# Kernel optimization log

Hardware: AMD Instinct MI355X
Metric: run time of the kernel (lower is better)

Reference implementation:

```python
import jax, jax.numpy as jnp
import numpy as np

B, S, T = 4, 1024, 1024
CTX, QIN, C, H = 1024, 1024, 1024, 16
HD = C // H  # per-head channels


def setup_inputs() -> dict:
    key = jax.random.key(0)
    ks = jax.random.split(key, 12)
    s = 0.02
    return {
        "query": jax.random.normal(ks[0], (B, S, QIN), jnp.float32),
        "key": jax.random.normal(ks[1], (B, T, CTX), jnp.float32),
        "value": jax.random.normal(ks[2], (B, T, CTX), jnp.float32),
        "mask": jax.random.randint(ks[3], (B, S, T), 0, 2).astype(bool),
        "Wq": jax.random.normal(ks[4], (C, QIN), jnp.float32) * s,
        "bq": jax.random.normal(ks[5], (C,), jnp.float32) * s,
        "Wk": jax.random.normal(ks[6], (C, CTX), jnp.float32) * s,
        "bk": jax.random.normal(ks[7], (C,), jnp.float32) * s,
        "Wv": jax.random.normal(ks[8], (C, CTX), jnp.float32) * s,
        "bv": jax.random.normal(ks[9], (C,), jnp.float32) * s,
        "Wo": jax.random.normal(ks[10], (C, C), jnp.float32) * s,
        "bo": jax.random.normal(ks[11], (C,), jnp.float32) * s,
    }


def reference(query, key, value, mask, Wq, bq, Wk, bk, Wv, bv, Wo, bo):
    b, s, _ = query.shape
    t = key.shape[1]
    c = Wq.shape[0]
    h, hd = H, c // H
    q = (query @ Wq.T + bq).reshape(b, s, h, hd)
    k = (key @ Wk.T + bk).reshape(b, t, h, hd)
    v = (value @ Wv.T + bv).reshape(b, t, h, hd)
    # [B,H,S,T] scores, scaled by 1/sqrt(head_dim)
    score = jnp.einsum('bshd,bthd->bhst', q, k) * (hd ** -0.5)
    # masked_fill_(~mask[:, None, 0:1], -inf): mask key positions via row 0
    score = jnp.where(mask[:, None, 0:1], score, -jnp.inf)
    weights = jax.nn.softmax(score, axis=-1)
    out = jnp.einsum('bhst,bthd->bshd', weights, v).reshape(b, s, c)
    out = out @ Wo.T + bo
    out = out * mask[..., 0:1].astype(out.dtype)
    return out
```

## Files before the change

### kernel.cpp

```cpp
#include <hip/hip_runtime.h>
#include <stdint.h>

#define Bb  4
#define Ss  1024
#define Tt  1024
#define Cc  1024
#define Hh  16
#define HDd 64
#define Kk  1024

typedef __bf16 bf16;
typedef __bf16 bf16x8 __attribute__((ext_vector_type(8)));
typedef float  f32x4  __attribute__((ext_vector_type(4)));
typedef __attribute__((address_space(1))) uint32_t gu32;
typedef __attribute__((address_space(3))) uint32_t lu32;

__device__ __forceinline__ void load_lds16(const bf16* g, bf16* l) {
    __builtin_amdgcn_global_load_lds((gu32*)g, (lu32*)l, 16, 0, 0);
}

#define BARRIER_LDS() do {                                    \
    asm volatile("s_waitcnt lgkmcnt(0)" ::: "memory");        \
    __builtin_amdgcn_s_barrier();                             \
} while (0)

#define BARRIER_VM() do {                                     \
    asm volatile("s_waitcnt vmcnt(0)" ::: "memory");          \
    __builtin_amdgcn_s_barrier();                             \
} while (0)

__global__ void cvt8(const float* __restrict__ s0, const float* __restrict__ s1,
                     const float* __restrict__ s2, const float* __restrict__ s3,
                     const float* __restrict__ s4, const float* __restrict__ s5,
                     const float* __restrict__ s6,
                     bf16* __restrict__ d0, bf16* __restrict__ d1,
                     bf16* __restrict__ d2, bf16* __restrict__ d3,
                     bf16* __restrict__ d4, bf16* __restrict__ d5,
                     bf16* __restrict__ d6)
{
    const float* s; bf16* d; int n;
    switch (blockIdx.y) {
        case 0: s = s0; d = d0; n = Bb * Ss * Kk; break;
        case 1: s = s1; d = d1; n = Bb * Ss * Kk; break;
        case 2: s = s2; d = d2; n = Bb * Ss * Kk; break;
        case 3: s = s3; d = d3; n = Cc * Kk; break;
        case 4: s = s4; d = d4; n = Cc * Kk; break;
        case 5: s = s5; d = d5; n = Cc * Kk; break;
        default: s = s6; d = d6; n = Cc * Kk; break;
    }
    const int i = (blockIdx.x * blockDim.x + threadIdx.x) * 8;
    if (i >= n) return;
    const float4 a = *(const float4*)(s + i);
    const float4 c = *(const float4*)(s + i + 4);
    bf16x8 o;
    o[0] = (bf16)a.x; o[1] = (bf16)a.y; o[2] = (bf16)a.z; o[3] = (bf16)a.w;
    o[4] = (bf16)c.x; o[5] = (bf16)c.y; o[6] = (bf16)c.z; o[7] = (bf16)c.w;
    *(bf16x8*)(d + i) = o;
}

__device__ __forceinline__ void mainloop_128x64_pf(
    const bf16* __restrict__ Ab, const bf16* __restrict__ Wb,
    bf16* As, bf16* Bs, f32x4 acc[4][2])
{
    const int tid  = threadIdx.x;
    const int wid  = tid >> 6;
    const int lane = tid & 63;
    const int l16  = lane & 15;
    const int quad = lane >> 4;
    const int wm   = wid >> 1;
    const int wn   = wid & 1;
    const int r8   = lane >> 3;
    const int ssw  = ((lane & 7) ^ r8) * 8;

    auto stage = [&](int k0) {
#pragma unroll
        for (int p = 0; p < 4; p++) {
            const int rb = wid * 32 + p * 8;
            load_lds16(Ab + (size_t)(rb + r8) * Kk + k0 + ssw, As + rb * 64);
        }
#pragma unroll
        for (int p = 0; p < 2; p++) {
            const int rb = wid * 16 + p * 8;
            load_lds16(Wb + (size_t)(rb + r8) * Kk + k0 + ssw, Bs + rb * 64);
        }
    };

    stage(0);
    BARRIER_VM();

    for (int k0 = 0; k0 < Kk; k0 += 64) {
        bf16x8 af[2][4], bw[2][2];
#pragma unroll
        for (int kh = 0; kh < 2; kh++) {
#pragma unroll
            for (int i = 0; i < 4; i++)
                af[kh][i] = *(const bf16x8*)(As + (wm * 64 + i * 16 + l16) * 64 +
                                             (((kh * 4 + quad) ^ (l16 & 7)) * 8));
#pragma unroll
            for (int j = 0; j < 2; j++)
                bw[kh][j] = *(const bf16x8*)(Bs + (wn * 32 + j * 16 + l16) * 64 +
                                             (((kh * 4 + quad) ^ (l16 & 7)) * 8));
        }
        BARRIER_LDS();
        if (k0 + 64 < Kk) stage(k0 + 64);
#pragma unroll
        for (int kh = 0; kh < 2; kh++)
#pragma unroll
            for (int i = 0; i < 4; i++)
#pragma unroll
                for (int j = 0; j < 2; j++)
                    acc[i][j] = __builtin_amdgcn_mfma_f32_16x16x32_bf16(af[kh][i], bw[kh][j], acc[i][j], 0, 0, 0);
        BARRIER_VM();
    }
}

__global__ __launch_bounds__(256)
void gemm_qkv(const bf16* __restrict__ Aq, const bf16* __restrict__ Ak, const bf16* __restrict__ Av,
              const bf16* __restrict__ Wq, const bf16* __restrict__ Wk, const bf16* __restrict__ Wv,
              const float* __restrict__ bq, const float* __restrict__ bk, const float* __restrict__ bv,
              bf16* __restrict__ Oq, bf16* __restrict__ Ok, bf16* __restrict__ Ov)
{
    __shared__ __align__(16) bf16 As[128 * 64];
    __shared__ __align__(16) bf16 Bs[64 * 64];
    const int z = blockIdx.z;
    const bf16*  A    = (z == 0) ? Aq : (z == 1) ? Ak : Av;
    const bf16*  W    = (z == 0) ? Wq : (z == 1) ? Wk : Wv;
    const float* bias = (z == 0) ? bq : (z == 1) ? bk : bv;
    bf16*        O    = (z == 0) ? Oq : (z == 1) ? Ok : Ov;

    f32x4 acc[4][2];
    const f32x4 z4 = {0.f, 0.f, 0.f, 0.f};
#pragma unroll
    for (int i = 0; i < 4; i++)
#pragma unroll
        for (int j = 0; j < 2; j++) acc[i][j] = z4;

    mainloop_128x64_pf(A + (size_t)blockIdx.x * 128 * Kk,
                       W + (size_t)blockIdx.y * 64 * Kk, As, Bs, acc);

    const int tid = threadIdx.x;
    const int wid = tid >> 6, lane = tid & 63;
    const int l16 = lane & 15, quad = lane >> 4;
    const int wm = wid >> 1, wn = wid & 1;
    const int row0 = blockIdx.x * 128 + wm * 64;
    const int col0 = blockIdx.y * 64 + wn * 32;
#pragma unroll
    for (int j = 0; j < 2; j++) {
        const int col = col0 + j * 16 + l16;
        const float bj = bias[col];
        const int h = col >> 6, d = col & 63;
#pragma unroll
        for (int i = 0; i < 4; i++) {
#pragma unroll
            for (int r = 0; r < 4; r++) {
                const int row = row0 + i * 16 + quad * 4 + r;
                const int b = row >> 10, s = row & 1023;
                const bf16 val = (bf16)(acc[i][j][r] + bj);
                if (z == 2) {
                    Ov[((size_t)((b * Hh + h) * HDd + d)) * Tt + s] = val;
                } else {
                    O[((size_t)(b * Hh + h) * Ss + s) * HDd + d] = val;
                }
            }
        }
    }
}

__global__ __launch_bounds__(256)
void gemm_out(const bf16* __restrict__ A, const bf16* __restrict__ W,
              const float* __restrict__ bias, const int* __restrict__ mask,
              float* __restrict__ out)
{
    __shared__ __align__(16) bf16 As[128 * 64];
    __shared__ __align__(16) bf16 Bs[64 * 64];
    f32x4 acc[4][2];
    const f32x4 z4 = {0.f, 0.f, 0.f, 0.f};
#pragma unroll
    for (int i = 0; i < 4; i++)
#pragma unroll
        for (int j = 0; j < 2; j++) acc[i][j] = z4;

    mainloop_128x64_pf(A + (size_t)blockIdx.x * 128 * Kk,
                       W + (size_t)blockIdx.y * 64 * Kk, As, Bs, acc);

    const int tid = threadIdx.x;
    const int wid = tid >> 6, lane = tid & 63;
    const int l16 = lane & 15, quad = lane >> 4;
    const int wm = wid >> 1, wn = wid & 1;
    const int row0 = blockIdx.x * 128 + wm * 64;
    const int col0 = blockIdx.y * 64 + wn * 32;
#pragma unroll
    for (int j = 0; j < 2; j++) {
        const int col = col0 + j * 16 + l16;
        const float bj = bias[col];
#pragma unroll
        for (int i = 0; i < 4; i++) {
#pragma unroll
            for (int r = 0; r < 4; r++) {
                const int row = row0 + i * 16 + quad * 4 + r;
                const float mval = (mask[(size_t)row * Tt] != 0) ? 1.f : 0.f;
                out[(size_t)row * Cc + col] = (acc[i][j][r] + bj) * mval;
            }
        }
    }
}

__global__ __launch_bounds__(256, 4)
void attn(const bf16* __restrict__ Q, const bf16* __restrict__ Kp, const bf16* __restrict__ Vt,
          const int* __restrict__ mask, bf16* __restrict__ X)
{
    __shared__ __align__(16) bf16 Ks[64 * 64];
    __shared__ __align__(16) bf16 Vs[64 * 64];
    __shared__ __align__(16) bf16 Ps[4][16 * 72];
    const int g   = blockIdx.x;
    const int xcd = g & 7, idx = g >> 3;
    const int bh  = xcd * 8 + (idx >> 4);
    const int qblk = idx & 15;
    const int b = bh >> 4, h = bh & 15;
    const int tid = threadIdx.x, wid = tid >> 6, lane = tid & 63;
    const int l16 = lane & 15, quad = lane >> 4;
    const bf16* Qbh = Q  + (size_t)bh * Ss * HDd;
    const bf16* Kbh = Kp + (size_t)bh * Tt * HDd;
    const bf16* Vbh = Vt + (size_t)bh * HDd * Tt;
    const int*  mb  = mask + (size_t)b * Ss * Tt;
    const int q0 = qblk * 64 + wid * 16;
    bf16* Psw = &Ps[wid][0];

    const bf16x8 qf0 = *(const bf16x8*)(Qbh + (size_t)(q0 + l16) * HDd + quad * 8);
    const bf16x8 qf1 = *(const bf16x8*)(Qbh + (size_t)(q0 + l16) * HDd + 32 + quad * 8);

    float ls[4];
    f32x4 o[4];
    const f32x4 z4 = {0.f, 0.f, 0.f, 0.f};
#pragma unroll
    for (int r = 0; r < 4; r++) ls[r] = 0.f;
#pragma unroll
    for (int dblk = 0; dblk < 4; dblk++) o[dblk] = z4;

    const int srow = lane >> 3;
    const int schk = lane & 7;
    const int sswz = (schk ^ srow) * 8;
    const int c80 = wid * 2, c81 = wid * 2 + 1;

    const bf16* kg0 = Kbh + (size_t)(c80 * 8 + srow) * HDd + sswz;
    const bf16* kg1 = Kbh + (size_t)(c81 * 8 + srow) * HDd + sswz;
    const bf16* vg0 = Vbh + (size_t)(c80 * 8 + srow) * Tt + sswz;
    const bf16* vg1 = Vbh + (size_t)(c81 * 8 + srow) * Tt + sswz;
    bf16* kd0 = Ks + c80 * 512 + lane * 8;
    bf16* kd1 = Ks + c81 * 512 + lane * 8;
    bf16* vd0 = Vs + c80 * 512 + lane * 8;
    bf16* vd1 = Vs + c81 * 512 + lane * 8;

    bf16x8 ka0, ka1, va0, va1;
    bf16x8 kb0, kb1, vb0, vb1;
    int mA0, mA1, mA2, mA3, mB0, mB1, mB2, mB3;

#define LOADA(KT) do { const int _kt = (KT);                          \
    ka0 = *(const bf16x8*)(kg0 + (size_t)_kt * HDd);                  \
    ka1 = *(const bf16x8*)(kg1 + (size_t)_kt * HDd);                  \
    va0 = *(const bf16x8*)(vg0 + _kt);                                \
    va1 = *(const bf16x8*)(vg1 + _kt);                                \
    mA0 = mb[_kt + l16];      mA1 = mb[_kt + 16 + l16];               \
    mA2 = mb[_kt + 32 + l16]; mA3 = mb[_kt + 48 + l16]; } while (0)
#define LOADB(KT) do { const int _kt = (KT);                          \
    kb0 = *(const bf16x8*)(kg0 + (size_t)_kt * HDd);                  \
    kb1 = *(const bf16x8*)(kg1 + (size_t)_kt * HDd);                  \
    vb0 = *(const bf16x8*)(vg0 + _kt);                                \
    vb1 = *(const bf16x8*)(vg1 + _kt);                                \
    mB0 = mb[_kt + l16];      mB1 = mb[_kt + 16 + l16];               \
    mB2 = mb[_kt + 32 + l16]; mB3 = mb[_kt + 48 + l16]; } while (0)
#define STOREA() do {                                                 \
    *(bf16x8*)kd0 = ka0; *(bf16x8*)kd1 = ka1;                         \
    *(bf16x8*)vd0 = va0; *(bf16x8*)vd1 = va1; } while (0)
#define STOREB() do {                                                 \
    *(bf16x8*)kd0 = kb0; *(bf16x8*)kd1 = kb1;                         \
    *(bf16x8*)vd0 = vb0; *(bf16x8*)vd1 = vb1; } while (0)

    auto compute = [&](int m0, int m1, int m2, int m3) {
        f32x4 sc[4];
#pragma unroll
        for (int nb = 0; nb < 4; nb++) sc[nb] = z4;
#pragma unroll
        for (int nb = 0; nb < 4; nb++) {
            const bf16* krow = Ks + (nb * 16 + l16) * 64;
            const bf16x8 kf0 = *(const bf16x8*)(krow + ((quad       ^ (l16 & 7)) * 8));
            const bf16x8 kf1 = *(const bf16x8*)(krow + (((4 + quad) ^ (l16 & 7)) * 8));
            sc[nb] = __builtin_amdgcn_mfma_f32_16x16x32_bf16(qf0, kf0, sc[nb], 0, 0, 0);
            sc[nb] = __builtin_amdgcn_mfma_f32_16x16x32_bf16(qf1, kf1, sc[nb], 0, 0, 0);
        }

        const int mm[4] = {m0, m1, m2, m3};
#pragma unroll
        for (int nb = 0; nb < 4; nb++) {
            const float madd = mm[nb] ? 0.f : -1e30f;
#pragma unroll
            for (int r = 0; r < 4; r++) {
                const float p = __expf(sc[nb][r] * 0.125f + madd);
                ls[r] += p;
                Psw[(quad * 4 + r) * 72 + nb * 16 + l16] = (bf16)p;
            }
        }

#pragma unroll
        for (int kh = 0; kh < 2; kh++) {
            const bf16x8 pf = *(const bf16x8*)(Psw + l16 * 72 + kh * 32 + quad * 8);
#pragma unroll
            for (int dblk = 0; dblk < 4; dblk++) {
                const bf16x8 vf = *(const bf16x8*)(Vs + (dblk * 16 + l16) * 64 +
                                                   (((kh * 4 + quad) ^ (l16 & 7)) * 8));
                o[dblk] = __builtin_amdgcn_mfma_f32_16x16x32_bf16(pf, vf, o[dblk], 0, 0, 0);
            }
        }
    };

    LOADA(0);

    for (int kt = 0; kt < Tt; kt += 128) {
        BARRIER_LDS();
        LOADB(kt + 64);
        STOREA();
        BARRIER_LDS();
        compute(mA0, mA1, mA2, mA3);

        BARRIER_LDS();
        LOADA((kt + 128 < Tt) ? (kt + 128) : (Tt - 64));
        STOREB();
        BARRIER_LDS();
        compute(mB0, mB1, mB2, mB3);
    }
#undef LOADA
#undef LOADB
#undef STOREA
#undef STOREB

#pragma unroll
    for (int off = 1; off <= 8; off <<= 1)
#pragma unroll
        for (int r = 0; r < 4; r++)
            ls[r] += __shfl_xor(ls[r], off, 64);
    float inv[4];
#pragma unroll
    for (int r = 0; r < 4; r++) inv[r] = 1.f / ls[r];

#pragma unroll
    for (int dblk = 0; dblk < 4; dblk++) {
#pragma unroll
        for (int r = 0; r < 4; r++) {
            const int srow_q = q0 + quad * 4 + r;
            const int d = dblk * 16 + l16;
            X[(size_t)(b * Ss + srow_q) * Cc + h * HDd + d] = (bf16)(o[dblk][r] * inv[r]);
        }
    }
}

extern "C" void kernel_launch(void* const* d_in, const int* in_sizes, int n_in,
                              void* d_out, int out_size, void* d_ws, size_t ws_size,
                              hipStream_t stream)
{
    const float* query = (const float*)d_in[0];
    const float* key   = (const float*)d_in[1];
    const float* value = (const float*)d_in[2];
    const int*   mask  = (const int*)d_in[3];
    const float* Wq = (const float*)d_in[4];
    const float* bq = (const float*)d_in[5];
    const float* Wk = (const float*)d_in[6];
    const float* bk = (const float*)d_in[7];
    const float* Wv = (const float*)d_in[8];
    const float* bv = (const float*)d_in[9];
    const float* Wo = (const float*)d_in[10];
    const float* bo = (const float*)d_in[11];
    float* out = (float*)d_out;

    char* ws = (char*)d_ws;
    const size_t MB = 1024 * 1024;
    bf16* qb  = (bf16*)(ws + 0 * MB);
    bf16* kb  = (bf16*)(ws + 8 * MB);
    bf16* vb  = (bf16*)(ws + 16 * MB);
    bf16* wqb = (bf16*)(ws + 24 * MB);
    bf16* wkb = (bf16*)(ws + 26 * MB);
    bf16* wvb = (bf16*)(ws + 28 * MB);
    bf16* wob = (bf16*)(ws + 30 * MB);
    bf16* Qp  = (bf16*)(ws + 32 * MB);
    bf16* Kpp = (bf16*)(ws + 40 * MB);
    bf16* Vtp = (bf16*)(ws + 48 * MB);
    bf16* Xb  = (bf16*)(ws + 56 * MB);

    cvt8<<<dim3(2048, 7), 256, 0, stream>>>(query, key, value, Wq, Wk, Wv, Wo,
                                            qb, kb, vb, wqb, wkb, wvb, wob);
    gemm_qkv<<<dim3(32, 16, 3), 256, 0, stream>>>(qb, kb, vb, wqb, wkb, wvb,
                                                  bq, bk, bv, Qp, Kpp, Vtp);
    attn<<<dim3(1024), 256, 0, stream>>>(Qp, Kpp, Vtp, mask, Xb);
    gemm_out<<<dim3(32, 16), 256, 0, stream>>>(Xb, wob, bo, mask, out);
}
```

Before: 223.1 us.

## Process two query sub-tiles per wave in attention to reuse K/V tiles

Each attention wave now handles 32 query rows instead of 16, so a block covers 128 queries and the grid halves to 512 blocks. Each K and V fragment loaded from LDS feeds two MFMAs, and the global K/V/mask traffic per query is halved. The cost is more registers (launch bounds drop to 2 blocks per SIMD set), a larger P scratch in LDS, and fewer blocks to spread over the CUs.

```diff
diff --git a/kernel.cpp b/kernel.cpp
--- a/kernel.cpp
+++ b/kernel.cpp
@@ -205,17 +205,17 @@
     }
 }
 
-__global__ __launch_bounds__(256, 4)
+__global__ __launch_bounds__(256, 2)
 void attn(const bf16* __restrict__ Q, const bf16* __restrict__ Kp, const bf16* __restrict__ Vt,
           const int* __restrict__ mask, bf16* __restrict__ X)
 {
     __shared__ __align__(16) bf16 Ks[64 * 64];
     __shared__ __align__(16) bf16 Vs[64 * 64];
-    __shared__ __align__(16) bf16 Ps[4][16 * 72];
+    __shared__ __align__(16) bf16 Ps[4][32 * 72];
     const int g   = blockIdx.x;
     const int xcd = g & 7, idx = g >> 3;
-    const int bh  = xcd * 8 + (idx >> 4);
-    const int qblk = idx & 15;
+    const int bh  = xcd * 8 + (idx >> 3);
+    const int qblk = idx & 7;
     const int b = bh >> 4, h = bh & 15;
     const int tid = threadIdx.x, wid = tid >> 6, lane = tid & 63;
     const int l16 = lane & 15, quad = lane >> 4;
@@ -223,19 +223,27 @@
     const bf16* Kbh = Kp + (size_t)bh * Tt * HDd;
     const bf16* Vbh = Vt + (size_t)bh * HDd * Tt;
     const int*  mb  = mask + (size_t)b * Ss * Tt;
-    const int q0 = qblk * 64 + wid * 16;
+    const int q0 = qblk * 128 + wid * 32;
     bf16* Psw = &Ps[wid][0];
 
-    const bf16x8 qf0 = *(const bf16x8*)(Qbh + (size_t)(q0 + l16) * HDd + quad * 8);
-    const bf16x8 qf1 = *(const bf16x8*)(Qbh + (size_t)(q0 + l16) * HDd + 32 + quad * 8);
-
-    float ls[4];
-    f32x4 o[4];
+    bf16x8 qf[2][2];
+#pragma unroll
+    for (int u = 0; u < 2; u++) {
+        qf[u][0] = *(const bf16x8*)(Qbh + (size_t)(q0 + u * 16 + l16) * HDd + quad * 8);
+        qf[u][1] = *(const bf16x8*)(Qbh + (size_t)(q0 + u * 16 + l16) * HDd + 32 + quad * 8);
+    }
+
+    float ls[2][4];
+    f32x4 o[2][4];
     const f32x4 z4 = {0.f, 0.f, 0.f, 0.f};
 #pragma unroll
-    for (int r = 0; r < 4; r++) ls[r] = 0.f;
-#pragma unroll
-    for (int dblk = 0; dblk < 4; dblk++) o[dblk] = z4;
+    for (int u = 0; u < 2; u++)
+#pragma unroll
+        for (int r = 0; r < 4; r++) ls[u][r] = 0.f;
+#pragma unroll
+    for (int u = 0; u < 2; u++)
+#pragma unroll
+        for (int dblk = 0; dblk < 4; dblk++) o[u][dblk] = z4;
 
     const int srow = lane >> 3;
     const int schk = lane & 7;
@@ -277,16 +285,21 @@
     *(bf16x8*)vd0 = vb0; *(bf16x8*)vd1 = vb1; } while (0)
 
     auto compute = [&](int m0, int m1, int m2, int m3) {
-        f32x4 sc[4];
-#pragma unroll
-        for (int nb = 0; nb < 4; nb++) sc[nb] = z4;
+        f32x4 sc[2][4];
+#pragma unroll
+        for (int u = 0; u < 2; u++)
+#pragma unroll
+            for (int nb = 0; nb < 4; nb++) sc[u][nb] = z4;
 #pragma unroll
         for (int nb = 0; nb < 4; nb++) {
             const bf16* krow = Ks + (nb * 16 + l16) * 64;
             const bf16x8 kf0 = *(const bf16x8*)(krow + ((quad       ^ (l16 & 7)) * 8));
             const bf16x8 kf1 = *(const bf16x8*)(krow + (((4 + quad) ^ (l16 & 7)) * 8));
-            sc[nb] = __builtin_amdgcn_mfma_f32_16x16x32_bf16(qf0, kf0, sc[nb], 0, 0, 0);
-            sc[nb] = __builtin_amdgcn_mfma_f32_16x16x32_bf16(qf1, kf1, sc[nb], 0, 0, 0);
+#pragma unroll
+            for (int u = 0; u < 2; u++) {
+                sc[u][nb] = __builtin_amdgcn_mfma_f32_16x16x32_bf16(qf[u][0], kf0, sc[u][nb], 0, 0, 0);
+                sc[u][nb] = __builtin_amdgcn_mfma_f32_16x16x32_bf16(qf[u][1], kf1, sc[u][nb], 0, 0, 0);
+            }
         }
 
         const int mm[4] = {m0, m1, m2, m3};
@@ -294,21 +307,26 @@
         for (int nb = 0; nb < 4; nb++) {
             const float madd = mm[nb] ? 0.f : -1e30f;
 #pragma unroll
-            for (int r = 0; r < 4; r++) {
-                const float p = __expf(sc[nb][r] * 0.125f + madd);
-                ls[r] += p;
-                Psw[(quad * 4 + r) * 72 + nb * 16 + l16] = (bf16)p;
+            for (int u = 0; u < 2; u++) {
+#pragma unroll
+                for (int r = 0; r < 4; r++) {
+                    const float p = __expf(sc[u][nb][r] * 0.125f + madd);
+                    ls[u][r] += p;
+                    Psw[(u * 16 + quad * 4 + r) * 72 + nb * 16 + l16] = (bf16)p;
+                }
             }
         }
 
 #pragma unroll
         for (int kh = 0; kh < 2; kh++) {
-            const bf16x8 pf = *(const bf16x8*)(Psw + l16 * 72 + kh * 32 + quad * 8);
+            const bf16x8 pf0 = *(const bf16x8*)(Psw + (l16) * 72 + kh * 32 + quad * 8);
+            const bf16x8 pf1 = *(const bf16x8*)(Psw + (16 + l16) * 72 + kh * 32 + quad * 8);
 #pragma unroll
             for (int dblk = 0; dblk < 4; dblk++) {
                 const bf16x8 vf = *(const bf16x8*)(Vs + (dblk * 16 + l16) * 64 +
                                                    (((kh * 4 + quad) ^ (l16 & 7)) * 8));
-                o[dblk] = __builtin_amdgcn_mfma_f32_16x16x32_bf16(pf, vf, o[dblk], 0, 0, 0);
+                o[0][dblk] = __builtin_amdgcn_mfma_f32_16x16x32_bf16(pf0, vf, o[0][dblk], 0, 0, 0);
+                o[1][dblk] = __builtin_amdgcn_mfma_f32_16x16x32_bf16(pf1, vf, o[1][dblk], 0, 0, 0);
             }
         }
     };
@@ -336,19 +354,26 @@
 #pragma unroll
     for (int off = 1; off <= 8; off <<= 1)
 #pragma unroll
-        for (int r = 0; r < 4; r++)
-            ls[r] += __shfl_xor(ls[r], off, 64);
-    float inv[4];
-#pragma unroll
-    for (int r = 0; r < 4; r++) inv[r] = 1.f / ls[r];
-
-#pragma unroll
-    for (int dblk = 0; dblk < 4; dblk++) {
-#pragma unroll
-        for (int r = 0; r < 4; r++) {
-            const int srow_q = q0 + quad * 4 + r;
-            const int d = dblk * 16 + l16;
-            X[(size_t)(b * Ss + srow_q) * Cc + h * HDd + d] = (bf16)(o[dblk][r] * inv[r]);
+        for (int u = 0; u < 2; u++)
+#pragma unroll
+            for (int r = 0; r < 4; r++)
+                ls[u][r] += __shfl_xor(ls[u][r], off, 64);
+    float inv[2][4];
+#pragma unroll
+    for (int u = 0; u < 2; u++)
+#pragma unroll
+        for (int r = 0; r < 4; r++) inv[u][r] = 1.f / ls[u][r];
+
+#pragma unroll
+    for (int u = 0; u < 2; u++) {
+#pragma unroll
+        for (int dblk = 0; dblk < 4; dblk++) {
+#pragma unroll
+            for (int r = 0; r < 4; r++) {
+                const int srow_q = q0 + u * 16 + quad * 4 + r;
+                const int d = dblk * 16 + l16;
+                X[(size_t)(b * Ss + srow_q) * Cc + h * HDd + d] = (bf16)(o[u][dblk][r] * inv[u][r]);
+            }
         }
     }
 }
@@ -389,6 +414,6 @@
                                             qb, kb, vb, wqb, wkb, wvb, wob);
     gemm_qkv<<<dim3(32, 16, 3), 256, 0, stream>>>(qb, kb, vb, wqb, wkb, wvb,
                                                   bq, bk, bv, Qp, Kpp, Vtp);
-    attn<<<dim3(1024), 256, 0, stream>>>(Qp, Kpp, Vtp, mask, Xb);
+    attn<<<dim3(512), 256, 0, stream>>>(Qp, Kpp, Vtp, mask, Xb);
     gemm_out<<<dim3(32, 16), 256, 0, stream>>>(Xb, wob, bo, mask, out);
 }
```

After: 221.1 us. Within noise of the previous version (-0.9%).
